# Kernel optimization log

Measured on AMD Instinct MI355X. Metric: run time of the kernel, lower is better.

The kernel has to match this reference:

```python
import jax, jax.numpy as jnp
import numpy as np
from jax import lax

B, T, I, H, O = 256, 128, 512, 1024, 512


def setup_inputs() -> dict:
    key = jax.random.key(0)
    ks = jax.random.split(key, 7)
    s = 1.0 / np.sqrt(H)  # PyTorch LSTM/Linear init bound
    x = jax.random.normal(ks[0], (B, T, I), dtype=jnp.float32)
    W_ih = jax.random.uniform(ks[1], (4 * H, I), jnp.float32, -s, s)
    W_hh = jax.random.uniform(ks[2], (4 * H, H), jnp.float32, -s, s)
    b_ih = jax.random.uniform(ks[3], (4 * H,), jnp.float32, -s, s)
    b_hh = jax.random.uniform(ks[4], (4 * H,), jnp.float32, -s, s)
    W_fc = jax.random.uniform(ks[5], (O, H), jnp.float32, -s, s)
    b_fc = jax.random.uniform(ks[6], (O,), jnp.float32, -s, s)
    return {"x": x, "W_ih": W_ih, "W_hh": W_hh, "b_ih": b_ih,
            "b_hh": b_hh, "W_fc": W_fc, "b_fc": b_fc}


def _lstm_last(x, W_ih, W_hh, b_ih, b_hh):
    # Precompute input contribution for all timesteps: [T, B, 4H]
    pre = jnp.einsum('bti,gi->tbg', x, W_ih) + b_ih + b_hh

    def step(carry, xg):
        h, c = carry
        gates = xg + h @ W_hh.T  # [B, 4H]
        i, f, g, o = jnp.split(gates, 4, axis=-1)  # PyTorch gate order i,f,g,o
        c = jax.nn.sigmoid(f) * c + jax.nn.sigmoid(i) * jnp.tanh(g)
        h = jax.nn.sigmoid(o) * jnp.tanh(c)
        return (h, c), None

    h0 = jnp.zeros((x.shape[0], W_hh.shape[1]), x.dtype)
    (h, c), _ = lax.scan(step, (h0, h0), pre)
    return h, c


def reference(x, W_ih, W_hh, b_ih, b_hh, W_fc, b_fc):
    h, c = _lstm_last(x, W_ih, W_hh, b_ih, b_hh)
    out = h @ W_fc.T + b_fc  # fc on last timestep hidden
    # hidden returned as (h_n, c_n) with leading n_layers=1 dim, as in PyTorch
    return out, (h[None], c[None])
```

## Files before the change

kernel.cpp:

```cpp
#include <hip/hip_runtime.h>

typedef short bf8 __attribute__((ext_vector_type(8)));
typedef float f32x4 __attribute__((ext_vector_type(4)));
typedef uint u32x4 __attribute__((ext_vector_type(4)));

static constexpr int BB = 256;
static constexpr int TT = 128;
static constexpr int II = 512;
static constexpr int HH = 1024;
static constexpr int OO = 512;
static constexpr int G4 = 4096;

static constexpr size_t OUT_H = (size_t)BB * OO;
static constexpr size_t OUT_C = OUT_H + (size_t)BB * HH;
static constexpr size_t HBUF  = (size_t)BB * HH;

__device__ __forceinline__ float bf2f(ushort u) {
    unsigned v = ((unsigned)u) << 16;
    return __builtin_bit_cast(float, v);
}
__device__ __forceinline__ ushort f2bf(float f) {
    unsigned x = __builtin_bit_cast(unsigned, f);
    x = x + 0x7FFFu + ((x >> 16) & 1u);
    return (ushort)(x >> 16);
}
__device__ __forceinline__ float sigf(float x) { return 1.0f / (1.0f + __expf(-x)); }
__device__ __forceinline__ float tanhf_(float x) { return 2.0f * sigf(2.0f * x) - 1.0f; }

__device__ __forceinline__ void st_wt_short(const ushort* p, uint v) {
    asm volatile("global_store_short %0, %1, off sc0 sc1" :: "v"(p), "v"(v) : "memory");
}
__device__ __forceinline__ void st_wt_b64(const ushort* p, uint2 v) {
    asm volatile("global_store_dwordx2 %0, %1, off sc0 sc1" :: "v"(p), "v"(v) : "memory");
}
__device__ __forceinline__ void st_wt_b128(const ushort* p, u32x4 v) {
    asm volatile("global_store_dwordx4 %0, %1, off sc0 sc1" :: "v"(p), "v"(v) : "memory");
}
__device__ __forceinline__ void ld_bp_ushort_issue(uint& dst, const ushort* p) {
    asm volatile("global_load_ushort %0, %1, off sc0 sc1" : "=v"(dst) : "v"(p) : "memory");
}
__device__ __forceinline__ void ld_bp_b128_issue(u32x4& dst, const ushort* p) {
    asm volatile("global_load_dwordx4 %0, %1, off sc0 sc1" : "=v"(dst) : "v"(p) : "memory");
}
__device__ __forceinline__ void wait_vm0() {
    asm volatile("s_waitcnt vmcnt(0)" ::: "memory");
    __builtin_amdgcn_sched_barrier(0);
}
#define WAITVM(N) do { asm volatile("s_waitcnt vmcnt(" #N ")" ::: "memory"); \
                       __builtin_amdgcn_sched_barrier(0); } while (0)

__device__ __forceinline__ void lightbar(int* slots, int bg, int gen) {
    asm volatile("s_waitcnt vmcnt(0) lgkmcnt(0)" ::: "memory");
    __builtin_amdgcn_sched_barrier(0);
    __syncthreads();
    int tid = threadIdx.x;
    if (tid == 0)
        asm volatile("global_store_dword %0, %1, off sc0 sc1" :: "v"(slots + bg * 32), "v"(gen) : "memory");
    if (tid < 64) {
        const int* sp = slots + tid * 32;
        int v;
        do {
            asm volatile("global_load_dword %0, %1, off sc0 sc1\n\ts_waitcnt vmcnt(0)"
                         : "=v"(v) : "v"(sp) : "memory");
            if (v >= gen) break;
            __builtin_amdgcn_s_sleep(1);
        } while (true);
    }
    __syncthreads();
}

__global__ void k_init(int* flags) {
    int i = blockIdx.x * 256 + threadIdx.x;
    if (i < 8192) flags[i] = 0;
}

__global__ void k_cast(const float* __restrict__ src, ushort* __restrict__ dst, int n4) {
    int i = blockIdx.x * blockDim.x + threadIdx.x;
    int stride = gridDim.x * blockDim.x;
    for (; i < n4; i += stride) {
        float4 v = ((const float4*)src)[i];
        ushort4 o;
        o.x = f2bf(v.x); o.y = f2bf(v.y); o.z = f2bf(v.z); o.w = f2bf(v.w);
        ((ushort4*)dst)[i] = o;
    }
}

__global__ void k_prep_w(const float* __restrict__ w, ushort* __restrict__ wp,
                         const float* __restrict__ bi, const float* __restrict__ bh,
                         float* __restrict__ bp, int Kdim) {
    int p = blockIdx.x;
    int orig = ((p >> 4) & 3) * HH + ((p >> 6) << 4) + (p & 15);
    const float* src = w + (size_t)orig * Kdim;
    ushort* dst = wp + (size_t)p * Kdim;
    for (int k = threadIdx.x; k < Kdim; k += 256) dst[k] = f2bf(src[k]);
    if (threadIdx.x == 0 && bp) bp[p] = bi[orig] + bh[orig];
}

__global__ __launch_bounds__(256) void k_main(
    const float* __restrict__ x, const ushort* __restrict__ wpih,
    const float* __restrict__ bp, ushort* __restrict__ pre,
    const ushort* __restrict__ wphh, ushort* __restrict__ hbf,
    float* __restrict__ dout, int* flags, int SEG) {
    __shared__ ushort wl[32 * 2048];
    __shared__ ushort Al[64 * 32];
    __shared__ ushort Bl[128 * 32];

    int tid = threadIdx.x;
    int bid = blockIdx.x;
    int g = bid >> 6, j = bid & 63;
    int row0 = g << 6;
    int* slots = flags + g * 2048;
    int gen = 0;
    int nseg = TT / SEG;

    int w = tid >> 6, l = tid & 63;
    int l15 = l & 15, kg = l >> 4;
    int wbase = ((l15 << 6) + (kg << 4)) ^ ((l15 & 7) << 4);

    {
        const ushort* wsrc = wphh + (size_t)(j << 6) * HH;
        for (int s = 0; s < 32; ++s) {
            int cidx = (s << 8) + tid;
            int c = cidx >> 7;
            int kc = cidx & 127;
            uint4 v = *(const uint4*)(wsrc + (size_t)c * HH + (kc << 3));
            int byte = ((kc >> 2) << 12) + ((((c << 6) + ((kc & 3) << 4))) ^ ((c & 7) << 4));
            *(uint4*)((char*)wl + byte) = v;
        }
        int r = tid >> 2, hc = (tid & 3) << 2;
        uint2 z; z.x = 0; z.y = 0;
        st_wt_b64(hbf + (size_t)(row0 + r) * HH + (j << 4) + hc, z);
    }

    int wm = w >> 1, wn = w & 1;
    int r0 = tid >> 2, kk = tid & 3;
    int sbyteA = ((r0 << 6) + (kk << 4)) ^ ((r0 & 7) << 4);
    int sbyteB1 = sbyteA + 4096;

    const ushort* hbase = hbf + (size_t)(row0 + (w << 4) + l15) * HH + (kg << 3);
    int drow = row0 + (w << 4) + (kg << 2);
    int hcol = (j << 4) + l15;
    const ushort* pbase = pre + (size_t)drow * G4 + (j << 6) + l15;
    float creg[4] = {0.f, 0.f, 0.f, 0.f};

    for (int sg = 0; sg < nseg; ++sg) {
        int t0 = sg * SEG;
        int ntiles = SEG << 5;
        for (int q = j; q < ntiles; q += 64) {
            int trel = q >> 5;
            int t = t0 + trel;
            int n0 = (q & 31) << 7;
            const float* xa = x + ((size_t)(row0 + r0) * TT + t) * II + (kk << 3);
            const ushort* gb0 = wpih + (size_t)(n0 + r0) * II + (kk << 3);
            const ushort* gb1 = gb0 + (size_t)64 * II;
            f32x4 acc[2][4];
#pragma unroll
            for (int mi = 0; mi < 2; ++mi)
#pragma unroll
                for (int ni = 0; ni < 4; ++ni) acc[mi][ni] = f32x4{0.f, 0.f, 0.f, 0.f};
            float4 a0 = *(const float4*)xa;
            float4 a1 = *(const float4*)(xa + 4);
            uint4 b0v = *(const uint4*)gb0;
            uint4 b1v = *(const uint4*)gb1;
            for (int ko = 0; ko < 16; ++ko) {
                union { ushort us[8]; uint4 v; } pa;
                pa.us[0] = f2bf(a0.x); pa.us[1] = f2bf(a0.y); pa.us[2] = f2bf(a0.z); pa.us[3] = f2bf(a0.w);
                pa.us[4] = f2bf(a1.x); pa.us[5] = f2bf(a1.y); pa.us[6] = f2bf(a1.z); pa.us[7] = f2bf(a1.w);
                __syncthreads();
                *(uint4*)((char*)Al + sbyteA) = pa.v;
                *(uint4*)((char*)Bl + sbyteA) = b0v;
                *(uint4*)((char*)Bl + sbyteB1) = b1v;
                __syncthreads();
                if (ko < 15) {
                    int k = (ko + 1) << 5;
                    a0 = *(const float4*)(xa + k);
                    a1 = *(const float4*)(xa + k + 4);
                    b0v = *(const uint4*)(gb0 + k);
                    b1v = *(const uint4*)(gb1 + k);
                }
                bf8 af[2], bv[4];
#pragma unroll
                for (int mi = 0; mi < 2; ++mi)
                    af[mi] = *(const bf8*)((char*)Al + wm * 2048 + mi * 1024 + wbase);
#pragma unroll
                for (int ni = 0; ni < 4; ++ni)
                    bv[ni] = *(const bf8*)((char*)Bl + wn * 4096 + ni * 1024 + wbase);
#pragma unroll
                for (int mi = 0; mi < 2; ++mi)
#pragma unroll
                    for (int ni = 0; ni < 4; ++ni)
                        acc[mi][ni] = __builtin_amdgcn_mfma_f32_16x16x32_bf16(af[mi], bv[ni], acc[mi][ni], 0, 0, 0);
            }
#pragma unroll
            for (int ni = 0; ni < 4; ++ni) {
                int col = n0 + wn * 64 + ni * 16 + l15;
                float bias = bp[col];
#pragma unroll
                for (int mi = 0; mi < 2; ++mi) {
                    int arow = row0 + wm * 32 + mi * 16 + (kg << 2);
#pragma unroll
                    for (int r = 0; r < 4; ++r)
                        st_wt_short(pre + ((size_t)trel * BB + arow + r) * G4 + col,
                                    (uint)f2bf(acc[mi][ni][r] + bias));
                }
            }
        }
        gen++; lightbar(slots, j, gen);

        uint prn[16];
#pragma unroll
        for (int ni = 0; ni < 4; ++ni)
#pragma unroll
            for (int r = 0; r < 4; ++r)
                ld_bp_ushort_issue(prn[ni * 4 + r], pbase + (size_t)r * G4 + (ni << 4));
        wait_vm0();

        for (int trel = 0; trel < SEG; ++trel) {
            int t = t0 + trel;
            const ushort* hr = hbase + (size_t)(t & 1) * HBUF;
            u32x4 xv[8], yv[8];

#define ISSUE8(B, C) \
            _Pragma("unroll") \
            for (int u = 0; u < 8; ++u) ld_bp_b128_issue(B[u], hr + (((C) * 8 + u) << 5));
#define CONSUME8(B, C) \
            _Pragma("unroll") \
            for (int u = 0; u < 8; ++u) { \
                int ko = (C) * 8 + u; \
                bf8 a = __builtin_bit_cast(bf8, B[u]); \
                _Pragma("unroll") \
                for (int ni = 0; ni < 4; ++ni) { \
                    bf8 b = *(const bf8*)((char*)wl + ko * 4096 + ni * 1024 + wbase); \
                    acc[ni] = __builtin_amdgcn_mfma_f32_16x16x32_bf16(a, b, acc[ni], 0, 0, 0); \
                } \
            }

            f32x4 acc[4];
            ISSUE8(xv, 0)
            ISSUE8(yv, 1)
#pragma unroll
            for (int ni = 0; ni < 4; ++ni)
#pragma unroll
                for (int r = 0; r < 4; ++r) acc[ni][r] = bf2f((ushort)prn[ni * 4 + r]);
            WAITVM(8);
            CONSUME8(xv, 0)
            ISSUE8(xv, 2)
            WAITVM(8);
            CONSUME8(yv, 1)
            ISSUE8(yv, 3)
            WAITVM(8);
            CONSUME8(xv, 2)
            {
                int nrel = (trel + 1 < SEG) ? trel + 1 : 0;
                const ushort* pnn = pre + ((size_t)nrel * BB + drow) * G4 + (j << 6) + l15;
#pragma unroll
                for (int ni = 0; ni < 4; ++ni)
#pragma unroll
                    for (int r = 0; r < 4; ++r)
                        ld_bp_ushort_issue(prn[ni * 4 + r], pnn + (size_t)r * G4 + (ni << 4));
            }
            WAITVM(16);
            CONSUME8(yv, 3)
#undef ISSUE8
#undef CONSUME8

            bool last = (t == TT - 1);
#pragma unroll
            for (int r = 0; r < 4; ++r) {
                float ig = sigf(acc[0][r]);
                float fg = sigf(acc[1][r]);
                float gg = tanhf_(acc[2][r]);
                float og = sigf(acc[3][r]);
                float c = fg * creg[r] + ig * gg;
                creg[r] = c;
                float h = og * tanhf_(c);
                Al[((w << 4) + (kg << 2) + r) * 16 + l15] = f2bf(h);
                if (last) {
                    dout[OUT_H + (size_t)(drow + r) * HH + hcol] = h;
                    dout[OUT_C + (size_t)(drow + r) * HH + hcol] = c;
                }
            }
            __syncthreads();
            if (tid < 128) {
                u32x4 v = *(const u32x4*)(Al + (tid << 3));
                const ushort* hop = hbf + (size_t)((t & 1) ^ 1) * HBUF
                                    + (size_t)(row0 + (tid >> 1)) * HH + (j << 4) + ((tid & 1) << 3);
                st_wt_b128(hop, v);
            }
            gen++; lightbar(slots, j, gen);
        }
    }
}

__global__ __launch_bounds__(256) void k_fc(const ushort* __restrict__ hlast,
                                            const ushort* __restrict__ wfc,
                                            const float* __restrict__ bfc,
                                            float* __restrict__ out) {
    int tid = threadIdx.x;
    int b0 = (blockIdx.x >> 3) << 6;
    int n0 = (blockIdx.x & 7) << 6;
    int w = tid >> 6, l = tid & 63;
    int l15 = l & 15, kg = l >> 4;
    const ushort* ha = hlast + (size_t)(b0 + (w << 4) + l15) * HH + (kg << 3);
    f32x4 acc[4];
#pragma unroll
    for (int ni = 0; ni < 4; ++ni) acc[ni] = f32x4{0.f, 0.f, 0.f, 0.f};
    for (int ko = 0; ko < 32; ++ko) {
        bf8 a = *(const bf8*)(ha + (ko << 5));
#pragma unroll
        for (int ni = 0; ni < 4; ++ni) {
            bf8 b = *(const bf8*)(wfc + (size_t)(n0 + ni * 16 + l15) * HH + (ko << 5) + (kg << 3));
            acc[ni] = __builtin_amdgcn_mfma_f32_16x16x32_bf16(a, b, acc[ni], 0, 0, 0);
        }
    }
    int drow = b0 + (w << 4) + (kg << 2);
#pragma unroll
    for (int ni = 0; ni < 4; ++ni) {
        int col = n0 + ni * 16 + l15;
        float bias = bfc[col];
#pragma unroll
        for (int r = 0; r < 4; ++r)
            out[(size_t)(drow + r) * OO + col] = acc[ni][r] + bias;
    }
}

extern "C" void kernel_launch(void* const* d_in, const int* in_sizes, int n_in,
                              void* d_out, int out_size, void* d_ws, size_t ws_size,
                              hipStream_t stream) {
    const float* x   = (const float*)d_in[0];
    const float* Wih = (const float*)d_in[1];
    const float* Whh = (const float*)d_in[2];
    const float* bih = (const float*)d_in[3];
    const float* bhh = (const float*)d_in[4];
    const float* Wfc = (const float*)d_in[5];
    const float* bfc = (const float*)d_in[6];
    float* out = (float*)d_out;

    char* ws = (char*)d_ws;
    size_t off = 0;
    ushort* wpih = (ushort*)(ws + off); off += (size_t)G4 * II * 2;
    ushort* wphh = (ushort*)(ws + off); off += (size_t)G4 * HH * 2;
    ushort* wfcb = (ushort*)(ws + off); off += (size_t)OO * HH * 2;
    float*  bp   = (float*)(ws + off);  off += (size_t)G4 * 4;
    int*    flags= (int*)(ws + off);    off += 8192 * 4;
    ushort* hbf  = (ushort*)(ws + off); off += (size_t)2 * BB * HH * 2;
    size_t fixed = off;
    int SEG = 16;
    while (SEG > 1 && fixed + (size_t)SEG * BB * G4 * 2 > ws_size) SEG >>= 1;
    ushort* pre = (ushort*)(ws + fixed);

    k_init<<<32, 256, 0, stream>>>(flags);
    k_cast<<<256, 256, 0, stream>>>(Wfc, wfcb, OO * HH / 4);
    k_prep_w<<<G4, 256, 0, stream>>>(Wih, wpih, bih, bhh, bp, II);
    k_prep_w<<<G4, 256, 0, stream>>>(Whh, wphh, nullptr, nullptr, nullptr, HH);
    k_main<<<256, 256, 0, stream>>>(x, wpih, bp, pre, wphh, hbf, out, flags, SEG);
    k_fc<<<32, 256, 0, stream>>>(hbf, wfcb, bfc, out);
}
```

Measured before the change: 1.544 ms.

## Split persistent LSTM across 512 blocks with 128-block group barriers

Doubles the persistent grid from 256 to 512 blocks, so each block owns 8 hidden units (32 gate columns) instead of 16. Per-block W_hh LDS shrinks to half and the kernel asks for two blocks per CU. The gate layout is reordered so that i/f and g/o halves sit in lanes 8 apart and are exchanged with shuffles. The barrier now spans 128 blocks per batch group, which cuts per-step MFMA and LDS work per block but doubles the number of participants each step must wait on.

```diff
diff --git a/kernel.cpp b/kernel.cpp
--- a/kernel.cpp
+++ b/kernel.cpp
@@ -30,9 +30,6 @@
 __device__ __forceinline__ void st_wt_short(const ushort* p, uint v) {
     asm volatile("global_store_short %0, %1, off sc0 sc1" :: "v"(p), "v"(v) : "memory");
 }
-__device__ __forceinline__ void st_wt_b64(const ushort* p, uint2 v) {
-    asm volatile("global_store_dwordx2 %0, %1, off sc0 sc1" :: "v"(p), "v"(v) : "memory");
-}
 __device__ __forceinline__ void st_wt_b128(const ushort* p, u32x4 v) {
     asm volatile("global_store_dwordx4 %0, %1, off sc0 sc1" :: "v"(p), "v"(v) : "memory");
 }
@@ -49,7 +46,7 @@
 #define WAITVM(N) do { asm volatile("s_waitcnt vmcnt(" #N ")" ::: "memory"); \
                        __builtin_amdgcn_sched_barrier(0); } while (0)
 
-__device__ __forceinline__ void lightbar(int* slots, int bg, int gen) {
+__device__ __forceinline__ void lightbar128(int* slots, int bg, int gen) {
     asm volatile("s_waitcnt vmcnt(0) lgkmcnt(0)" ::: "memory");
     __builtin_amdgcn_sched_barrier(0);
     __syncthreads();
@@ -57,21 +54,24 @@
     if (tid == 0)
         asm volatile("global_store_dword %0, %1, off sc0 sc1" :: "v"(slots + bg * 32), "v"(gen) : "memory");
     if (tid < 64) {
-        const int* sp = slots + tid * 32;
-        int v;
-        do {
-            asm volatile("global_load_dword %0, %1, off sc0 sc1\n\ts_waitcnt vmcnt(0)"
-                         : "=v"(v) : "v"(sp) : "memory");
-            if (v >= gen) break;
+        const int* p1 = slots + tid * 32;
+        const int* p2 = slots + (tid + 64) * 32;
+        int v1, v2;
+        for (;;) {
+            asm volatile("global_load_dword %0, %2, off sc0 sc1\n\t"
+                         "global_load_dword %1, %3, off sc0 sc1\n\t"
+                         "s_waitcnt vmcnt(0)"
+                         : "=v"(v1), "=v"(v2) : "v"(p1), "v"(p2) : "memory");
+            if (__all(v1 >= gen && v2 >= gen)) break;
             __builtin_amdgcn_s_sleep(1);
-        } while (true);
+        }
     }
     __syncthreads();
 }
 
 __global__ void k_init(int* flags) {
     int i = blockIdx.x * 256 + threadIdx.x;
-    if (i < 8192) flags[i] = 0;
+    if (i < 16384) flags[i] = 0;
 }
 
 __global__ void k_cast(const float* __restrict__ src, ushort* __restrict__ dst, int n4) {
@@ -89,27 +89,30 @@
                          const float* __restrict__ bi, const float* __restrict__ bh,
                          float* __restrict__ bp, int Kdim) {
     int p = blockIdx.x;
-    int orig = ((p >> 4) & 3) * HH + ((p >> 6) << 4) + (p & 15);
+    int jj = p >> 5, n = (p >> 4) & 1, c = p & 15;
+    int gate = (n << 1) | (c >> 3);
+    int orig = gate * HH + (jj << 3) + (c & 7);
     const float* src = w + (size_t)orig * Kdim;
     ushort* dst = wp + (size_t)p * Kdim;
     for (int k = threadIdx.x; k < Kdim; k += 256) dst[k] = f2bf(src[k]);
     if (threadIdx.x == 0 && bp) bp[p] = bi[orig] + bh[orig];
 }
 
-__global__ __launch_bounds__(256) void k_main(
+__global__ __launch_bounds__(256, 2) void k_main(
     const float* __restrict__ x, const ushort* __restrict__ wpih,
     const float* __restrict__ bp, ushort* __restrict__ pre,
     const ushort* __restrict__ wphh, ushort* __restrict__ hbf,
     float* __restrict__ dout, int* flags, int SEG) {
-    __shared__ ushort wl[32 * 2048];
+    __shared__ ushort wl[32 * 1024];
     __shared__ ushort Al[64 * 32];
     __shared__ ushort Bl[128 * 32];
 
     int tid = threadIdx.x;
     int bid = blockIdx.x;
-    int g = bid >> 6, j = bid & 63;
+    int g = ((bid >> 8) << 1) | ((bid >> 7) & 1);
+    int j = bid & 127;
     int row0 = g << 6;
-    int* slots = flags + g * 2048;
+    int* slots = flags + g * 4096;
     int gen = 0;
     int nseg = TT / SEG;
 
@@ -118,18 +121,19 @@
     int wbase = ((l15 << 6) + (kg << 4)) ^ ((l15 & 7) << 4);
 
     {
-        const ushort* wsrc = wphh + (size_t)(j << 6) * HH;
-        for (int s = 0; s < 32; ++s) {
+        const ushort* wsrc = wphh + (size_t)(j << 5) * HH;
+        for (int s = 0; s < 16; ++s) {
             int cidx = (s << 8) + tid;
             int c = cidx >> 7;
             int kc = cidx & 127;
             uint4 v = *(const uint4*)(wsrc + (size_t)c * HH + (kc << 3));
-            int byte = ((kc >> 2) << 12) + ((((c << 6) + ((kc & 3) << 4))) ^ ((c & 7) << 4));
+            int byte = ((kc >> 2) << 11) + ((((c << 6) + ((kc & 3) << 4))) ^ ((c & 7) << 4));
             *(uint4*)((char*)wl + byte) = v;
         }
-        int r = tid >> 2, hc = (tid & 3) << 2;
-        uint2 z; z.x = 0; z.y = 0;
-        st_wt_b64(hbf + (size_t)(row0 + r) * HH + (j << 4) + hc, z);
+        if (tid < 64) {
+            u32x4 z = {0, 0, 0, 0};
+            st_wt_b128(hbf + (size_t)(row0 + tid) * HH + (j << 3), z);
+        }
     }
 
     int wm = w >> 1, wn = w & 1;
@@ -139,14 +143,15 @@
 
     const ushort* hbase = hbf + (size_t)(row0 + (w << 4) + l15) * HH + (kg << 3);
     int drow = row0 + (w << 4) + (kg << 2);
-    int hcol = (j << 4) + l15;
-    const ushort* pbase = pre + (size_t)drow * G4 + (j << 6) + l15;
+    int hcol = (j << 3) + (l15 & 7);
+    bool hi = (l15 & 8) != 0;
+    const ushort* pbase = pre + (size_t)drow * G4 + (j << 5) + l15;
     float creg[4] = {0.f, 0.f, 0.f, 0.f};
 
     for (int sg = 0; sg < nseg; ++sg) {
         int t0 = sg * SEG;
         int ntiles = SEG << 5;
-        for (int q = j; q < ntiles; q += 64) {
+        for (int q = j; q < ntiles; q += 128) {
             int trel = q >> 5;
             int t = t0 + trel;
             int n0 = (q & 31) << 7;
@@ -205,14 +210,14 @@
                 }
             }
         }
-        gen++; lightbar(slots, j, gen);
-
-        uint prn[16];
-#pragma unroll
-        for (int ni = 0; ni < 4; ++ni)
+        gen++; lightbar128(slots, j, gen);
+
+        uint prn[8];
+#pragma unroll
+        for (int n = 0; n < 2; ++n)
 #pragma unroll
             for (int r = 0; r < 4; ++r)
-                ld_bp_ushort_issue(prn[ni * 4 + r], pbase + (size_t)r * G4 + (ni << 4));
+                ld_bp_ushort_issue(prn[n * 4 + r], pbase + (size_t)r * G4 + (n << 4));
         wait_vm0();
 
         for (int trel = 0; trel < SEG; ++trel) {
@@ -229,19 +234,19 @@
                 int ko = (C) * 8 + u; \
                 bf8 a = __builtin_bit_cast(bf8, B[u]); \
                 _Pragma("unroll") \
-                for (int ni = 0; ni < 4; ++ni) { \
-                    bf8 b = *(const bf8*)((char*)wl + ko * 4096 + ni * 1024 + wbase); \
-                    acc[ni] = __builtin_amdgcn_mfma_f32_16x16x32_bf16(a, b, acc[ni], 0, 0, 0); \
+                for (int n = 0; n < 2; ++n) { \
+                    bf8 b = *(const bf8*)((char*)wl + ko * 2048 + n * 1024 + wbase); \
+                    acc[n] = __builtin_amdgcn_mfma_f32_16x16x32_bf16(a, b, acc[n], 0, 0, 0); \
                 } \
             }
 
-            f32x4 acc[4];
+            f32x4 acc[2];
             ISSUE8(xv, 0)
             ISSUE8(yv, 1)
 #pragma unroll
-            for (int ni = 0; ni < 4; ++ni)
-#pragma unroll
-                for (int r = 0; r < 4; ++r) acc[ni][r] = bf2f((ushort)prn[ni * 4 + r]);
+            for (int n = 0; n < 2; ++n)
+#pragma unroll
+                for (int r = 0; r < 4; ++r) acc[n][r] = bf2f((ushort)prn[n * 4 + r]);
             WAITVM(8);
             CONSUME8(xv, 0)
             ISSUE8(xv, 2)
@@ -252,14 +257,14 @@
             CONSUME8(xv, 2)
             {
                 int nrel = (trel + 1 < SEG) ? trel + 1 : 0;
-                const ushort* pnn = pre + ((size_t)nrel * BB + drow) * G4 + (j << 6) + l15;
-#pragma unroll
-                for (int ni = 0; ni < 4; ++ni)
+                const ushort* pnn = pre + ((size_t)nrel * BB + drow) * G4 + (j << 5) + l15;
+#pragma unroll
+                for (int n = 0; n < 2; ++n)
 #pragma unroll
                     for (int r = 0; r < 4; ++r)
-                        ld_bp_ushort_issue(prn[ni * 4 + r], pnn + (size_t)r * G4 + (ni << 4));
-            }
-            WAITVM(16);
+                        ld_bp_ushort_issue(prn[n * 4 + r], pnn + (size_t)r * G4 + (n << 4));
+            }
+            WAITVM(8);
             CONSUME8(yv, 3)
 #undef ISSUE8
 #undef CONSUME8
@@ -267,27 +272,31 @@
             bool last = (t == TT - 1);
 #pragma unroll
             for (int r = 0; r < 4; ++r) {
-                float ig = sigf(acc[0][r]);
-                float fg = sigf(acc[1][r]);
-                float gg = tanhf_(acc[2][r]);
-                float og = sigf(acc[3][r]);
-                float c = fg * creg[r] + ig * gg;
+                float a0 = acc[0][r], a1 = acc[1][r];
+                float x0 = __shfl_xor(a0, 8);
+                float x1 = __shfl_xor(a1, 8);
+                float ig = hi ? x0 : a0;
+                float fg = hi ? a0 : x0;
+                float gg = hi ? x1 : a1;
+                float og = hi ? a1 : x1;
+                float c = sigf(fg) * creg[r] + sigf(ig) * tanhf_(gg);
                 creg[r] = c;
-                float h = og * tanhf_(c);
-                Al[((w << 4) + (kg << 2) + r) * 16 + l15] = f2bf(h);
-                if (last) {
-                    dout[OUT_H + (size_t)(drow + r) * HH + hcol] = h;
-                    dout[OUT_C + (size_t)(drow + r) * HH + hcol] = c;
+                float h = sigf(og) * tanhf_(c);
+                if (!hi) {
+                    Al[((w << 4) + (kg << 2) + r) * 8 + (l15 & 7)] = f2bf(h);
+                    if (last) {
+                        dout[OUT_H + (size_t)(drow + r) * HH + hcol] = h;
+                        dout[OUT_C + (size_t)(drow + r) * HH + hcol] = c;
+                    }
                 }
             }
             __syncthreads();
-            if (tid < 128) {
+            if (tid < 64) {
                 u32x4 v = *(const u32x4*)(Al + (tid << 3));
-                const ushort* hop = hbf + (size_t)((t & 1) ^ 1) * HBUF
-                                    + (size_t)(row0 + (tid >> 1)) * HH + (j << 4) + ((tid & 1) << 3);
-                st_wt_b128(hop, v);
-            }
-            gen++; lightbar(slots, j, gen);
+                st_wt_b128(hbf + (size_t)((t & 1) ^ 1) * HBUF
+                           + (size_t)(row0 + tid) * HH + (j << 3), v);
+            }
+            gen++; lightbar128(slots, j, gen);
         }
     }
 }
@@ -342,17 +351,17 @@
     ushort* wphh = (ushort*)(ws + off); off += (size_t)G4 * HH * 2;
     ushort* wfcb = (ushort*)(ws + off); off += (size_t)OO * HH * 2;
     float*  bp   = (float*)(ws + off);  off += (size_t)G4 * 4;
-    int*    flags= (int*)(ws + off);    off += 8192 * 4;
+    int*    flags= (int*)(ws + off);    off += 16384 * 4;
     ushort* hbf  = (ushort*)(ws + off); off += (size_t)2 * BB * HH * 2;
     size_t fixed = off;
     int SEG = 16;
     while (SEG > 1 && fixed + (size_t)SEG * BB * G4 * 2 > ws_size) SEG >>= 1;
     ushort* pre = (ushort*)(ws + fixed);
 
-    k_init<<<32, 256, 0, stream>>>(flags);
+    k_init<<<64, 256, 0, stream>>>(flags);
     k_cast<<<256, 256, 0, stream>>>(Wfc, wfcb, OO * HH / 4);
     k_prep_w<<<G4, 256, 0, stream>>>(Wih, wpih, bih, bhh, bp, II);
     k_prep_w<<<G4, 256, 0, stream>>>(Whh, wphh, nullptr, nullptr, nullptr, HH);
-    k_main<<<256, 256, 0, stream>>>(x, wpih, bp, pre, wphh, hbf, out, flags, SEG);
+    k_main<<<512, 256, 0, stream>>>(x, wpih, bp, pre, wphh, hbf, out, flags, SEG);
     k_fc<<<32, 256, 0, stream>>>(hbf, wfcb, bfc, out);
 }
```

New measurement: 1.839 ms. 1.19x slower.
